# Performance work log

Hardware: AMD Instinct MI355X
Metric: run time of the kernel (lower is better)

## Reference

```python
import jax, jax.numpy as jnp
import numpy as np

N = 100000   # nodes
E = 1200000  # edges
G = 512      # graphs in batch
H = 64       # hidden_dim
EED = 8      # edge_emb_dim
VOCABS = (120, 10, 7, 5, 2)
EDIMS = (64, 16, 8, 8, 4)
BN_EPS = 1e-5


def _lin(x, w, b):
    # torch nn.Linear: y = x @ W^T + b
    return x @ w.T + b


def setup_inputs() -> dict:
    key = jax.random.key(0)
    ks = iter(jax.random.split(key, 64))
    s = 0.02
    d = {}
    d["x"] = jax.random.randint(next(ks), (N, 5), 0, 120)
    d["edge_index"] = jax.random.randint(next(ks), (2, E), 0, N)
    d["edge_attr"] = jax.random.randint(next(ks), (E, 3), 0, 16)
    d["batch"] = jnp.sort(jax.random.randint(next(ks), (N,), 0, G))
    for i, (v, dd) in enumerate(zip(VOCABS, EDIMS)):
        d[f"emb{i}"] = jax.random.normal(next(ks), (v, dd), jnp.float32) * s
    d["proj_w"] = jax.random.normal(next(ks), (H, sum(EDIMS)), jnp.float32) * s
    d["proj_b"] = jnp.zeros((H,), jnp.float32)
    for i in (1, 2, 3):
        d[f"eemb{i}"] = jax.random.normal(next(ks), (16, EED), jnp.float32) * s
        d[f"lin_e{i}_w"] = jax.random.normal(next(ks), (H, EED), jnp.float32) * s
        d[f"lin_e{i}_b"] = jnp.zeros((H,), jnp.float32)
        d[f"eps{i}"] = jnp.zeros((), jnp.float32)
        d[f"mlp{i}_w1"] = jax.random.normal(next(ks), (H, H), jnp.float32) * s
        d[f"mlp{i}_b1"] = jnp.zeros((H,), jnp.float32)
        d[f"mlp{i}_w2"] = jax.random.normal(next(ks), (H, H), jnp.float32) * s
        d[f"mlp{i}_b2"] = jnp.zeros((H,), jnp.float32)
    d["bn_g"] = jnp.ones((H,), jnp.float32)
    d["bn_b"] = jnp.zeros((H,), jnp.float32)
    d["bn_rm"] = jnp.zeros((H,), jnp.float32)
    d["bn_rv"] = jnp.ones((H,), jnp.float32)
    d["gate_w"] = jax.random.normal(next(ks), (1, H), jnp.float32) * s
    d["gate_b"] = jnp.zeros((1,), jnp.float32)
    d["head_w1"] = jax.random.normal(next(ks), (128, H), jnp.float32) * s
    d["head_b1"] = jnp.zeros((128,), jnp.float32)
    d["head_w2"] = jax.random.normal(next(ks), (1, 128), jnp.float32) * s
    d["head_b2"] = jnp.zeros((1,), jnp.float32)
    return d


def reference(x, edge_index, edge_attr, batch,
              emb0, emb1, emb2, emb3, emb4, proj_w, proj_b,
              eemb1, lin_e1_w, lin_e1_b, eps1, mlp1_w1, mlp1_b1, mlp1_w2, mlp1_b2,
              eemb2, lin_e2_w, lin_e2_b, eps2, mlp2_w1, mlp2_b1, mlp2_w2, mlp2_b2,
              eemb3, lin_e3_w, lin_e3_b, eps3, mlp3_w1, mlp3_b1, mlp3_w2, mlp3_b2,
              bn_g, bn_b, bn_rm, bn_rv, gate_w, gate_b,
              head_w1, head_b1, head_w2, head_b2):
    # --- node embedding lookup (clamped per-table, as in torch) ---
    tabs = [emb0, emb1, emb2, emb3, emb4]
    feats = [t[jnp.clip(x[:, i], 0, t.shape[0] - 1)] for i, t in enumerate(tabs)]
    h = jnp.concatenate(feats, axis=-1)            # [N, 100]
    h = _lin(h, proj_w, proj_b)                    # [N, H]  (dropout = identity, eval)

    # --- edge hash, shared by all blocks ---
    eh = (edge_attr[:, 0] + 3 * edge_attr[:, 1] + 7 * edge_attr[:, 2]) % 16  # [E]
    src, dst = edge_index[0], edge_index[1]

    def gine(h, eemb, lw, lb, eps, w1, b1, w2, b2):
        # GINEConv: mlp((1+eps) x_i + sum_j relu(x_j + lin(e_ij)))
        e = _lin(eemb[eh], lw, lb)                        # [E, H]
        msg = jax.nn.relu(h[src] + e)                     # [E, H] gather + combine
        agg = jax.ops.segment_sum(msg, dst, num_segments=N)  # scatter-add to targets
        z = (1.0 + eps) * h + agg
        return _lin(jax.nn.relu(_lin(z, w1, b1)), w2, b2)

    h = jax.nn.relu(gine(h, eemb1, lin_e1_w, lin_e1_b, eps1, mlp1_w1, mlp1_b1, mlp1_w2, mlp1_b2))
    h = jax.nn.relu(gine(h, eemb2, lin_e2_w, lin_e2_b, eps2, mlp2_w1, mlp2_b1, mlp2_w2, mlp2_b2))
    h = jax.nn.relu(gine(h, eemb3, lin_e3_w, lin_e3_b, eps3, mlp3_w1, mlp3_b1, mlp3_w2, mlp3_b2))

    # BatchNorm1d (eval mode, running stats)
    h = (h - bn_rm) * jax.lax.rsqrt(bn_rv + BN_EPS) * bn_g + bn_b

    # AttentionalAggregation: segment softmax over gate, weighted segment sum
    gate = _lin(h, gate_w, gate_b)[:, 0]                  # [N]
    m = jax.ops.segment_max(gate, batch, num_segments=G)  # [G]
    w = jnp.exp(gate - m[batch])
    den = jax.ops.segment_sum(w, batch, num_segments=G) + 1e-16
    alpha = w / den[batch]                                # [N]
    graph = jax.ops.segment_sum(alpha[:, None] * h, batch, num_segments=G)  # [G, H]

    out = _lin(jax.nn.relu(_lin(graph, head_w1, head_b1)), head_w2, head_b2)  # [G, 1]
    return out[:, 0]
```

## Files before the change

kernel.cpp:

```cpp
#include <hip/hip_runtime.h>
#include <stdint.h>

#define N_NODES 100000
#define N_EDGES 1200000
#define N_GRAPH 512
#define HID 64

#define NBUCK 391
#define BCAP  4096
#define CHUNK 4096

#define PRE_JOBS (144 * 64 + 3 * 1024 + 64 + NBUCK)

__device__ __forceinline__ unsigned short f2bf(float f) {
    unsigned u = __float_as_uint(f);
    u += 0x7FFF + ((u >> 16) & 1);
    return (unsigned short)(u >> 16);
}
__device__ __forceinline__ float bf2f(unsigned short b) {
    return __uint_as_float((unsigned)b << 16);
}

__global__ __launch_bounds__(256) void k_pre(
    const float* emb0, const float* emb1, const float* emb2, const float* emb3, const float* emb4,
    const float* proj_w,
    const float* ee1, const float* lw1, const float* lb1,
    const float* ee2, const float* lw2, const float* lb2,
    const float* ee3, const float* lw3, const float* lb3,
    const float* bn_g, const float* bn_b, const float* bn_rm, const float* bn_rv,
    float* ptab, float* elin, float* bnsc, float* bnsh, int* cursor)
{
    int job = blockIdx.x * 256 + threadIdx.x;
    if (job < 144 * 64) {
        int row = job >> 6, c = job & 63;
        const float* emb; int lr, dim, off;
        if (row < 120)      { emb = emb0; lr = row;       dim = 64; off = 0;  }
        else if (row < 130) { emb = emb1; lr = row - 120; dim = 16; off = 64; }
        else if (row < 137) { emb = emb2; lr = row - 130; dim = 8;  off = 80; }
        else if (row < 142) { emb = emb3; lr = row - 137; dim = 8;  off = 88; }
        else                { emb = emb4; lr = row - 142; dim = 4;  off = 96; }
        float s = 0.f;
        for (int d = 0; d < dim; ++d)
            s += emb[lr * dim + d] * proj_w[c * 100 + off + d];
        ptab[row * 64 + c] = s;
    } else if (job < 144 * 64 + 3 * 1024) {
        int j = job - 144 * 64;
        int L = j >> 10; int r = (j >> 6) & 15; int c = j & 63;
        const float* ee = (L == 0) ? ee1 : (L == 1) ? ee2 : ee3;
        const float* lw = (L == 0) ? lw1 : (L == 1) ? lw2 : lw3;
        const float* lb = (L == 0) ? lb1 : (L == 1) ? lb2 : lb3;
        float s = lb[c];
        for (int d = 0; d < 8; ++d) s += ee[r * 8 + d] * lw[c * 8 + d];
        elin[j] = s;
    } else if (job < 144 * 64 + 3 * 1024 + 64) {
        int c = job - (144 * 64 + 3 * 1024);
        float sc = bn_g[c] * rsqrtf(bn_rv[c] + 1e-5f);
        bnsc[c] = sc;
        bnsh[c] = bn_b[c] - bn_rm[c] * sc;
    } else if (job < PRE_JOBS) {
        cursor[job - (144 * 64 + 3 * 1024 + 64)] = 0;
    }
}

__global__ __launch_bounds__(256) void k_embed(const int* x, const float* ptab,
                                               const float* proj_b, float* h,
                                               unsigned short* h2) {
    int id = blockIdx.x * 256 + threadIdx.x;
    if (id >= N_NODES * HID) return;
    int n = id >> 6, c = id & 63;
    const int* xr = x + n * 5;
    int r0 = min(max(xr[0], 0), 119);
    int r1 = 120 + min(max(xr[1], 0), 9);
    int r2 = 130 + min(max(xr[2], 0), 6);
    int r3 = 137 + min(max(xr[3], 0), 4);
    int r4 = 142 + min(max(xr[4], 0), 1);
    float v = proj_b[c] + ptab[r0 * 64 + c] + ptab[r1 * 64 + c] + ptab[r2 * 64 + c]
            + ptab[r3 * 64 + c] + ptab[r4 * 64 + c];
    h[id] = v;
    h2[id] = f2bf(v);
}

__global__ __launch_bounds__(256) void k_gptr(const int* batch, int* gptr) {
    int n = blockIdx.x * 256 + threadIdx.x;
    if (n >= N_NODES) return;
    int b = batch[n];
    int bp = (n == 0) ? -1 : batch[n - 1];
    for (int g = bp + 1; g <= b; ++g) gptr[g] = n;
    if (n == N_NODES - 1) {
        for (int g = b + 1; g <= N_GRAPH; ++g) gptr[g] = N_NODES;
    }
}

__global__ __launch_bounds__(256) void k_bin(const int* __restrict__ ei,
                                             const int* __restrict__ ea,
                                             int* __restrict__ cursor,
                                             int* __restrict__ binned) {
    __shared__ int pay[CHUNK];
    __shared__ unsigned short bkid[CHUNK];
    __shared__ int hist[NBUCK], inc[NBUCK], tmp[NBUCK], gdelta[NBUCK];
    int t = threadIdx.x;
    int e0 = blockIdx.x * CHUNK;
    for (int i = t; i < NBUCK; i += 256) hist[i] = 0;
    __syncthreads();
    int mypay[16], myrb[16];
    #pragma unroll
    for (int j = 0; j < 16; ++j) {
        int e = e0 + j * 256 + t;
        myrb[j] = -1;
        if (e < N_EDGES) {
            int s = ei[e];
            int d = ei[N_EDGES + e];
            int hsh = (ea[e * 3] + 3 * ea[e * 3 + 1] + 7 * ea[e * 3 + 2]) & 15;
            int b = d >> 8;
            mypay[j] = s | (hsh << 17) | ((d & 255) << 21);
            int r = atomicAdd(&hist[b], 1);
            myrb[j] = r | (b << 12);
        }
    }
    __syncthreads();
    for (int i = t; i < NBUCK; i += 256) inc[i] = hist[i];
    __syncthreads();
    for (int off = 1; off < NBUCK; off <<= 1) {
        for (int i = t; i < NBUCK; i += 256) tmp[i] = inc[i] + ((i >= off) ? inc[i - off] : 0);
        __syncthreads();
        for (int i = t; i < NBUCK; i += 256) inc[i] = tmp[i];
        __syncthreads();
    }
    for (int i = t; i < NBUCK; i += 256) {
        int c = hist[i];
        int gp = c ? atomicAdd(&cursor[i], c) : 0;
        gdelta[i] = i * BCAP + gp - (inc[i] - c);
    }
    __syncthreads();
    #pragma unroll
    for (int j = 0; j < 16; ++j) {
        if (myrb[j] >= 0) {
            int b = myrb[j] >> 12, r = myrb[j] & 0xFFF;
            int slot = (inc[b] - hist[b]) + r;
            pay[slot] = mypay[j];
            bkid[slot] = (unsigned short)b;
        }
    }
    __syncthreads();
    int tot = inc[NBUCK - 1];
    for (int i = t; i < tot; i += 256)
        binned[gdelta[bkid[i]] + i] = pay[i];
}

__global__ __launch_bounds__(512) void k_bscan(const int* cursor, int* bbase, int* rowptr) {
    __shared__ int s[512], tp[512];
    int t = threadIdx.x;
    int v = (t < NBUCK) ? cursor[t] : 0;
    s[t] = v;
    __syncthreads();
    for (int off = 1; off < 512; off <<= 1) {
        tp[t] = s[t] + ((t >= off) ? s[t - off] : 0);
        __syncthreads();
        s[t] = tp[t];
        __syncthreads();
    }
    if (t < NBUCK) bbase[t] = s[t] - v;
    if (t == 0) { bbase[NBUCK] = N_EDGES; rowptr[N_NODES] = N_EDGES; }
}

__global__ __launch_bounds__(256) void k_fin(const int* __restrict__ binned,
                                             const int* __restrict__ cursor,
                                             const int* __restrict__ bbase,
                                             int* __restrict__ rowptr,
                                             int* __restrict__ epk) {
    __shared__ int h2[256], sc[256], cur[256];
    int b = blockIdx.x, t = threadIdx.x;
    int cnt = cursor[b];
    int gb = bbase[b];
    int node0 = b << 8;
    h2[t] = 0;
    __syncthreads();
    const int* bp = binned + b * BCAP;
    for (int i = t; i < cnt; i += 256) atomicAdd(&h2[(bp[i] >> 21) & 255], 1);
    __syncthreads();
    sc[t] = h2[t];
    __syncthreads();
    for (int off = 1; off < 256; off <<= 1) {
        int v = (t >= off) ? sc[t - off] : 0;
        __syncthreads();
        sc[t] += v;
        __syncthreads();
    }
    int ex = sc[t] - h2[t];
    cur[t] = ex;
    int n = node0 + t;
    if (n < N_NODES) rowptr[n] = gb + ex;
    __syncthreads();
    for (int i = t; i < cnt; i += 256) {
        int p = bp[i];
        int pos = atomicAdd(&cur[(p >> 21) & 255], 1);
        epk[gb + pos] = p & 0x1FFFFF;
    }
}

__global__ __launch_bounds__(256) void k_gather(const unsigned short* __restrict__ h2,
                                                const float* __restrict__ elinL,
                                                const int* __restrict__ rowptr,
                                                const int* __restrict__ epk,
                                                float* __restrict__ agg) {
    __shared__ float es[16 * 64];
    int t = threadIdx.x;
    ((float4*)es)[t] = ((const float4*)elinL)[t];
    __syncthreads();
    int n = blockIdx.x * 4 + (t >> 6);
    if (n >= N_NODES) return;
    int lane = t & 63;
    int grp = lane >> 4;
    int c4 = (lane & 15) << 2;
    int p0 = rowptr[n], p1 = rowptr[n + 1];
    float4 acc = make_float4(0.f, 0.f, 0.f, 0.f);
    int p = p0 + grp;
    while (p + 4 < p1) {
        int pk0 = epk[p];
        int pk1 = epk[p + 4];
        ushort4 a0 = *(const ushort4*)(h2 + (pk0 & 0x1FFFF) * 64 + c4);
        ushort4 a1 = *(const ushort4*)(h2 + (pk1 & 0x1FFFF) * 64 + c4);
        float4 e0 = *(const float4*)(es + ((pk0 >> 17) & 15) * 64 + c4);
        float4 e1 = *(const float4*)(es + ((pk1 >> 17) & 15) * 64 + c4);
        acc.x += fmaxf(bf2f(a0.x) + e0.x, 0.f) + fmaxf(bf2f(a1.x) + e1.x, 0.f);
        acc.y += fmaxf(bf2f(a0.y) + e0.y, 0.f) + fmaxf(bf2f(a1.y) + e1.y, 0.f);
        acc.z += fmaxf(bf2f(a0.z) + e0.z, 0.f) + fmaxf(bf2f(a1.z) + e1.z, 0.f);
        acc.w += fmaxf(bf2f(a0.w) + e0.w, 0.f) + fmaxf(bf2f(a1.w) + e1.w, 0.f);
        p += 8;
    }
    if (p < p1) {
        int pk0 = epk[p];
        ushort4 a0 = *(const ushort4*)(h2 + (pk0 & 0x1FFFF) * 64 + c4);
        float4 e0 = *(const float4*)(es + ((pk0 >> 17) & 15) * 64 + c4);
        acc.x += fmaxf(bf2f(a0.x) + e0.x, 0.f);
        acc.y += fmaxf(bf2f(a0.y) + e0.y, 0.f);
        acc.z += fmaxf(bf2f(a0.z) + e0.z, 0.f);
        acc.w += fmaxf(bf2f(a0.w) + e0.w, 0.f);
    }
    acc.x += __shfl_down(acc.x, 32, 64);
    acc.y += __shfl_down(acc.y, 32, 64);
    acc.z += __shfl_down(acc.z, 32, 64);
    acc.w += __shfl_down(acc.w, 32, 64);
    acc.x += __shfl_down(acc.x, 16, 64);
    acc.y += __shfl_down(acc.y, 16, 64);
    acc.z += __shfl_down(acc.z, 16, 64);
    acc.w += __shfl_down(acc.w, 16, 64);
    if (grp == 0) *(float4*)(agg + n * 64 + c4) = acc;
}

__global__ __launch_bounds__(256) void k_mlp2(const float* __restrict__ hin,
                                              const float* __restrict__ agg,
                                              const float* __restrict__ epsp,
                                              const float* __restrict__ W1,
                                              const float* __restrict__ b1,
                                              const float* __restrict__ W2,
                                              const float* __restrict__ b2,
                                              float* __restrict__ out,
                                              unsigned short* __restrict__ h2out,
                                              const float* __restrict__ bnsc,
                                              const float* __restrict__ bnsh,
                                              const float* __restrict__ gate_w,
                                              const float* __restrict__ gate_b,
                                              float* __restrict__ gate) {
    __shared__ float in_s[64 * 68];
    __shared__ float wt_s[64 * 68];
    int t = threadIdx.x;
    int row0 = blockIdx.x * 64;
    float epsv = 1.f + epsp[0];
    for (int idx = t; idx < 1024; idx += 256) {
        int r = idx >> 4, cc4 = (idx & 15) << 2;
        int gr = row0 + r;
        float4 v = make_float4(0.f, 0.f, 0.f, 0.f);
        if (gr < N_NODES) {
            float4 a = *(const float4*)(hin + gr * 64 + cc4);
            float4 b = *(const float4*)(agg + gr * 64 + cc4);
            v.x = epsv * a.x + b.x; v.y = epsv * a.y + b.y;
            v.z = epsv * a.z + b.z; v.w = epsv * a.w + b.w;
        }
        *(float4*)(in_s + r * 68 + cc4) = v;
    }
    for (int idx = t; idx < 1024; idx += 256) {
        int cc = idx >> 4, k4 = (idx & 15) << 2;
        float4 w = *(const float4*)(W1 + cc * 64 + k4);
        wt_s[(k4 + 0) * 68 + cc] = w.x;
        wt_s[(k4 + 1) * 68 + cc] = w.y;
        wt_s[(k4 + 2) * 68 + cc] = w.z;
        wt_s[(k4 + 3) * 68 + cc] = w.w;
    }
    __syncthreads();
    int tc = t & 15, tr = t >> 4;
    float acc[4][4] = {};
    for (int k4 = 0; k4 < 16; ++k4) {
        float4 a[4], b[4];
        #pragma unroll
        for (int i = 0; i < 4; ++i) a[i] = *(float4*)(in_s + (tr + 16 * i) * 68 + k4 * 4);
        #pragma unroll
        for (int kk = 0; kk < 4; ++kk) b[kk] = *(float4*)(wt_s + (k4 * 4 + kk) * 68 + tc * 4);
        #pragma unroll
        for (int i = 0; i < 4; ++i) {
            float ax = a[i].x, ay = a[i].y, az = a[i].z, aw = a[i].w;
            acc[i][0] += ax * b[0].x + ay * b[1].x + az * b[2].x + aw * b[3].x;
            acc[i][1] += ax * b[0].y + ay * b[1].y + az * b[2].y + aw * b[3].y;
            acc[i][2] += ax * b[0].z + ay * b[1].z + az * b[2].z + aw * b[3].z;
            acc[i][3] += ax * b[0].w + ay * b[1].w + az * b[2].w + aw * b[3].w;
        }
    }
    __syncthreads();
    {
        float4 bb1 = *(const float4*)(b1 + tc * 4);
        #pragma unroll
        for (int i = 0; i < 4; ++i) {
            float* row = in_s + (tr + 16 * i) * 68 + tc * 4;
            row[0] = fmaxf(acc[i][0] + bb1.x, 0.f);
            row[1] = fmaxf(acc[i][1] + bb1.y, 0.f);
            row[2] = fmaxf(acc[i][2] + bb1.z, 0.f);
            row[3] = fmaxf(acc[i][3] + bb1.w, 0.f);
        }
    }
    for (int idx = t; idx < 1024; idx += 256) {
        int cc = idx >> 4, k4 = (idx & 15) << 2;
        float4 w = *(const float4*)(W2 + cc * 64 + k4);
        wt_s[(k4 + 0) * 68 + cc] = w.x;
        wt_s[(k4 + 1) * 68 + cc] = w.y;
        wt_s[(k4 + 2) * 68 + cc] = w.z;
        wt_s[(k4 + 3) * 68 + cc] = w.w;
    }
    __syncthreads();
    float acc2[4][4] = {};
    for (int k4 = 0; k4 < 16; ++k4) {
        float4 a[4], b[4];
        #pragma unroll
        for (int i = 0; i < 4; ++i) a[i] = *(float4*)(in_s + (tr + 16 * i) * 68 + k4 * 4);
        #pragma unroll
        for (int kk = 0; kk < 4; ++kk) b[kk] = *(float4*)(wt_s + (k4 * 4 + kk) * 68 + tc * 4);
        #pragma unroll
        for (int i = 0; i < 4; ++i) {
            float ax = a[i].x, ay = a[i].y, az = a[i].z, aw = a[i].w;
            acc2[i][0] += ax * b[0].x + ay * b[1].x + az * b[2].x + aw * b[3].x;
            acc2[i][1] += ax * b[0].y + ay * b[1].y + az * b[2].y + aw * b[3].y;
            acc2[i][2] += ax * b[0].z + ay * b[1].z + az * b[2].z + aw * b[3].z;
            acc2[i][3] += ax * b[0].w + ay * b[1].w + az * b[2].w + aw * b[3].w;
        }
    }
    float4 bb2 = *(const float4*)(b2 + tc * 4);
    if (gate == nullptr) {
        #pragma unroll
        for (int i = 0; i < 4; ++i) {
            int gr = row0 + tr + 16 * i;
            if (gr < N_NODES) {
                float4 o;
                o.x = fmaxf(acc2[i][0] + bb2.x, 0.f);
                o.y = fmaxf(acc2[i][1] + bb2.y, 0.f);
                o.z = fmaxf(acc2[i][2] + bb2.z, 0.f);
                o.w = fmaxf(acc2[i][3] + bb2.w, 0.f);
                *(float4*)(out + gr * 64 + tc * 4) = o;
                ushort4 ob;
                ob.x = f2bf(o.x); ob.y = f2bf(o.y); ob.z = f2bf(o.z); ob.w = f2bf(o.w);
                *(ushort4*)(h2out + gr * 64 + tc * 4) = ob;
            }
        }
    } else {
        float4 sc = *(const float4*)(bnsc + tc * 4);
        float4 sh = *(const float4*)(bnsh + tc * 4);
        float4 gw = *(const float4*)(gate_w + tc * 4);
        float gb = gate_b[0];
        #pragma unroll
        for (int i = 0; i < 4; ++i) {
            int gr = row0 + tr + 16 * i;
            float4 o;
            o.x = fmaxf(acc2[i][0] + bb2.x, 0.f) * sc.x + sh.x;
            o.y = fmaxf(acc2[i][1] + bb2.y, 0.f) * sc.y + sh.y;
            o.z = fmaxf(acc2[i][2] + bb2.z, 0.f) * sc.z + sh.z;
            o.w = fmaxf(acc2[i][3] + bb2.w, 0.f) * sc.w + sh.w;
            float p = o.x * gw.x + o.y * gw.y + o.z * gw.z + o.w * gw.w;
            p += __shfl_down(p, 8, 16);
            p += __shfl_down(p, 4, 16);
            p += __shfl_down(p, 2, 16);
            p += __shfl_down(p, 1, 16);
            if (gr < N_NODES) {
                *(float4*)(out + gr * 64 + tc * 4) = o;
                if (tc == 0) gate[gr] = p + gb;
            }
        }
    }
}

__global__ __launch_bounds__(256) void k_att(const float* __restrict__ h,
                                             const float* __restrict__ gate,
                                             const int* __restrict__ gptr,
                                             float* __restrict__ graph) {
    __shared__ float red[4];
    __shared__ float acc_s[4][64];
    __shared__ float m_s, den_s;
    int t = threadIdx.x, g = blockIdx.x;
    int n0 = gptr[g], n1 = gptr[g + 1];
    float m = -INFINITY;
    for (int n = n0 + t; n < n1; n += 256) m = fmaxf(m, gate[n]);
    #pragma unroll
    for (int off = 32; off > 0; off >>= 1) m = fmaxf(m, __shfl_down(m, off, 64));
    if ((t & 63) == 0) red[t >> 6] = m;
    __syncthreads();
    if (t == 0) m_s = fmaxf(fmaxf(red[0], red[1]), fmaxf(red[2], red[3]));
    __syncthreads();
    m = m_s;
    float s = 0.f;
    for (int n = n0 + t; n < n1; n += 256) s += expf(gate[n] - m);
    #pragma unroll
    for (int off = 32; off > 0; off >>= 1) s += __shfl_down(s, off, 64);
    if ((t & 63) == 0) red[t >> 6] = s;
    __syncthreads();
    if (t == 0) den_s = red[0] + red[1] + red[2] + red[3] + 1e-16f;
    __syncthreads();
    float invden = 1.f / den_s;
    int c = t & 63, w = t >> 6;
    float acc = 0.f;
    for (int n = n0 + w; n < n1; n += 4) {
        float a = expf(gate[n] - m);
        acc += a * h[n * 64 + c];
    }
    acc_s[w][c] = acc;
    __syncthreads();
    if (w == 0)
        graph[g * 64 + c] = (acc_s[0][c] + acc_s[1][c] + acc_s[2][c] + acc_s[3][c]) * invden;
}

__global__ __launch_bounds__(128) void k_head(const float* graph, const float* w1, const float* b1,
                                              const float* w2, const float* b2, float* out) {
    __shared__ float w1s[128 * 65];
    __shared__ float gs[64];
    __shared__ float red[2];
    int t = threadIdx.x, g = blockIdx.x;
    for (int idx = t; idx < 128 * 16; idx += 128) {
        int r = idx >> 4, c4 = (idx & 15) << 2;
        float4 v = *(const float4*)(w1 + r * 64 + c4);
        w1s[r * 65 + c4 + 0] = v.x;
        w1s[r * 65 + c4 + 1] = v.y;
        w1s[r * 65 + c4 + 2] = v.z;
        w1s[r * 65 + c4 + 3] = v.w;
    }
    if (t < 64) gs[t] = graph[g * 64 + t];
    __syncthreads();
    float s = b1[t];
    #pragma unroll
    for (int k = 0; k < 64; ++k) s += gs[k] * w1s[t * 65 + k];
    float p = fmaxf(s, 0.f) * w2[t];
    #pragma unroll
    for (int off = 32; off > 0; off >>= 1) p += __shfl_down(p, off, 64);
    if ((t & 63) == 0) red[t >> 6] = p;
    __syncthreads();
    if (t == 0) out[g] = red[0] + red[1] + b2[0];
}

extern "C" void kernel_launch(void* const* d_in, const int* in_sizes, int n_in,
                              void* d_out, int out_size, void* d_ws, size_t ws_size,
                              hipStream_t stream) {
    const int* x    = (const int*)d_in[0];
    const int* ei   = (const int*)d_in[1];
    const int* ea   = (const int*)d_in[2];
    const int* bat  = (const int*)d_in[3];
    const float* emb0 = (const float*)d_in[4];
    const float* emb1 = (const float*)d_in[5];
    const float* emb2 = (const float*)d_in[6];
    const float* emb3 = (const float*)d_in[7];
    const float* emb4 = (const float*)d_in[8];
    const float* proj_w = (const float*)d_in[9];
    const float* proj_b = (const float*)d_in[10];
    const float* bn_g  = (const float*)d_in[35];
    const float* bn_b  = (const float*)d_in[36];
    const float* bn_rm = (const float*)d_in[37];
    const float* bn_rv = (const float*)d_in[38];
    const float* gate_w = (const float*)d_in[39];
    const float* gate_b = (const float*)d_in[40];
    const float* head_w1 = (const float*)d_in[41];
    const float* head_b1 = (const float*)d_in[42];
    const float* head_w2 = (const float*)d_in[43];
    const float* head_b2 = (const float*)d_in[44];

    char* wsb = (char*)d_ws;
    size_t o = 0;
    auto alloc = [&](size_t bytes) -> void* {
        void* p = wsb + o;
        o += (bytes + 255) & ~(size_t)255;
        return p;
    };
    float* ptab   = (float*)alloc(144 * 64 * 4);
    float* elin   = (float*)alloc(3 * 16 * 64 * 4);
    float* bnsc   = (float*)alloc(64 * 4);
    float* bnsh   = (float*)alloc(64 * 4);
    int* cursor   = (int*)alloc(NBUCK * 4);
    int* bbase    = (int*)alloc((NBUCK + 1) * 4);
    int* gptr     = (int*)alloc((N_GRAPH + 1) * 4);
    int* rowptr   = (int*)alloc(((size_t)N_NODES + 1) * 4);
    int* binned   = (int*)alloc((size_t)NBUCK * BCAP * 4);
    int* epk      = (int*)alloc((size_t)N_EDGES * 4);
    float* h      = (float*)alloc((size_t)N_NODES * 64 * 4);
    unsigned short* h2 = (unsigned short*)alloc((size_t)N_NODES * 64 * 2);
    float* agg    = (float*)alloc((size_t)N_NODES * 64 * 4);
    float* gate   = (float*)alloc((size_t)N_NODES * 4);
    float* graph  = (float*)alloc((size_t)N_GRAPH * 64 * 4);

    k_pre<<<(PRE_JOBS + 255) / 256, 256, 0, stream>>>(
                                  emb0, emb1, emb2, emb3, emb4, proj_w,
                                  (const float*)d_in[11], (const float*)d_in[12], (const float*)d_in[13],
                                  (const float*)d_in[19], (const float*)d_in[20], (const float*)d_in[21],
                                  (const float*)d_in[27], (const float*)d_in[28], (const float*)d_in[29],
                                  bn_g, bn_b, bn_rm, bn_rv,
                                  ptab, elin, bnsc, bnsh, cursor);
    k_embed<<<(N_NODES * 64 + 255) / 256, 256, 0, stream>>>(x, ptab, proj_b, h, h2);
    k_gptr<<<(N_NODES + 255) / 256, 256, 0, stream>>>(bat, gptr);
    k_bin<<<(N_EDGES + CHUNK - 1) / CHUNK, 256, 0, stream>>>(ei, ea, cursor, binned);
    k_bscan<<<1, 512, 0, stream>>>(cursor, bbase, rowptr);
    k_fin<<<NBUCK, 256, 0, stream>>>(binned, cursor, bbase, rowptr, epk);

    for (int L = 0; L < 3; ++L) {
        const float* epsp = (const float*)d_in[14 + L * 8];
        const float* w1   = (const float*)d_in[15 + L * 8];
        const float* b1   = (const float*)d_in[16 + L * 8];
        const float* w2   = (const float*)d_in[17 + L * 8];
        const float* b2   = (const float*)d_in[18 + L * 8];
        k_gather<<<(N_NODES + 3) / 4, 256, 0, stream>>>(h2, elin + L * 1024, rowptr, epk, agg);
        if (L < 2) {
            k_mlp2<<<(N_NODES + 63) / 64, 256, 0, stream>>>(h, agg, epsp, w1, b1, w2, b2, h, h2,
                                                            nullptr, nullptr, nullptr, nullptr,
                                                            nullptr);
        } else {
            k_mlp2<<<(N_NODES + 63) / 64, 256, 0, stream>>>(h, agg, epsp, w1, b1, w2, b2, h, nullptr,
                                                            bnsc, bnsh, gate_w, gate_b, gate);
        }
    }

    k_att<<<N_GRAPH, 256, 0, stream>>>(h, gate, gptr, graph);
    k_head<<<N_GRAPH, 128, 0, stream>>>(graph, head_w1, head_b1, head_w2, head_b2, (float*)d_out);
}
```

Before: 474.4 us.

## Use bf16 MFMA for GIN MLPs, pre-convert weights, fuse head into attention

The per-layer two-layer MLP kernel is rewritten to use bf16 MFMA 16x16x32 instructions. Weights are converted to bf16 once in the prep kernel and held in registers, and the intermediate activations are staged in LDS as bf16. This replaces the fp32 FMA tiling and the weight transposes into shared memory. The separate head kernel is also folded into the attention pooling kernel to save a launch. The cost is lower precision in the MLP inputs and hidden activations, plus uncoalesced scalar output stores.

Result: faster. 445.3 us (-6.1%).

```diff
diff --git a/kernel.cpp b/kernel.cpp
--- a/kernel.cpp
+++ b/kernel.cpp
@@ -10,7 +10,11 @@
 #define BCAP  4096
 #define CHUNK 4096
 
-#define PRE_JOBS (144 * 64 + 3 * 1024 + 64 + NBUCK)
+#define PRE_W0  (144 * 64 + 3 * 1024 + 64 + NBUCK)
+#define PRE_JOBS (PRE_W0 + 6 * 4096)
+
+typedef __attribute__((ext_vector_type(8))) short bshort8;
+typedef __attribute__((ext_vector_type(4))) float f32x4;
 
 __device__ __forceinline__ unsigned short f2bf(float f) {
     unsigned u = __float_as_uint(f);
@@ -28,7 +32,10 @@
     const float* ee2, const float* lw2, const float* lb2,
     const float* ee3, const float* lw3, const float* lb3,
     const float* bn_g, const float* bn_b, const float* bn_rm, const float* bn_rv,
-    float* ptab, float* elin, float* bnsc, float* bnsh, int* cursor)
+    const float* w11, const float* w12, const float* w21, const float* w22,
+    const float* w31, const float* w32,
+    float* ptab, float* elin, float* bnsc, float* bnsh, int* cursor,
+    unsigned short* wbf)
 {
     int job = blockIdx.x * 256 + threadIdx.x;
     if (job < 144 * 64) {
@@ -57,8 +64,14 @@
         float sc = bn_g[c] * rsqrtf(bn_rv[c] + 1e-5f);
         bnsc[c] = sc;
         bnsh[c] = bn_b[c] - bn_rm[c] * sc;
+    } else if (job < PRE_W0) {
+        cursor[job - (144 * 64 + 3 * 1024 + 64)] = 0;
     } else if (job < PRE_JOBS) {
-        cursor[job - (144 * 64 + 3 * 1024 + 64)] = 0;
+        int j2 = job - PRE_W0;
+        int sel = j2 >> 12;
+        const float* W = (sel == 0) ? w11 : (sel == 1) ? w12 : (sel == 2) ? w21
+                       : (sel == 3) ? w22 : (sel == 4) ? w31 : w32;
+        wbf[j2] = f2bf(W[j2 & 4095]);
     }
 }
 
@@ -248,12 +261,12 @@
     if (grp == 0) *(float4*)(agg + n * 64 + c4) = acc;
 }
 
-__global__ __launch_bounds__(256) void k_mlp2(const float* __restrict__ hin,
+__global__ __launch_bounds__(256) void k_mlpm(const float* __restrict__ hin,
                                               const float* __restrict__ agg,
                                               const float* __restrict__ epsp,
-                                              const float* __restrict__ W1,
+                                              const unsigned short* __restrict__ wbf1,
                                               const float* __restrict__ b1,
-                                              const float* __restrict__ W2,
+                                              const unsigned short* __restrict__ wbf2,
                                               const float* __restrict__ b2,
                                               float* __restrict__ out,
                                               unsigned short* __restrict__ h2out,
@@ -262,125 +275,100 @@
                                               const float* __restrict__ gate_w,
                                               const float* __restrict__ gate_b,
                                               float* __restrict__ gate) {
-    __shared__ float in_s[64 * 68];
-    __shared__ float wt_s[64 * 68];
+    __shared__ unsigned short zb[64 * 72];
+    __shared__ unsigned short hb[64 * 72];
     int t = threadIdx.x;
     int row0 = blockIdx.x * 64;
     float epsv = 1.f + epsp[0];
     for (int idx = t; idx < 1024; idx += 256) {
-        int r = idx >> 4, cc4 = (idx & 15) << 2;
+        int r = idx >> 4, c4 = (idx & 15) << 2;
         int gr = row0 + r;
         float4 v = make_float4(0.f, 0.f, 0.f, 0.f);
         if (gr < N_NODES) {
-            float4 a = *(const float4*)(hin + gr * 64 + cc4);
-            float4 b = *(const float4*)(agg + gr * 64 + cc4);
+            float4 a = *(const float4*)(hin + gr * 64 + c4);
+            float4 b = *(const float4*)(agg + gr * 64 + c4);
             v.x = epsv * a.x + b.x; v.y = epsv * a.y + b.y;
             v.z = epsv * a.z + b.z; v.w = epsv * a.w + b.w;
         }
-        *(float4*)(in_s + r * 68 + cc4) = v;
-    }
-    for (int idx = t; idx < 1024; idx += 256) {
-        int cc = idx >> 4, k4 = (idx & 15) << 2;
-        float4 w = *(const float4*)(W1 + cc * 64 + k4);
-        wt_s[(k4 + 0) * 68 + cc] = w.x;
-        wt_s[(k4 + 1) * 68 + cc] = w.y;
-        wt_s[(k4 + 2) * 68 + cc] = w.z;
-        wt_s[(k4 + 3) * 68 + cc] = w.w;
-    }
-    __syncthreads();
-    int tc = t & 15, tr = t >> 4;
-    float acc[4][4] = {};
-    for (int k4 = 0; k4 < 16; ++k4) {
-        float4 a[4], b[4];
+        ushort4 zv;
+        zv.x = f2bf(v.x); zv.y = f2bf(v.y); zv.z = f2bf(v.z); zv.w = f2bf(v.w);
+        *(ushort4*)(zb + r * 72 + c4) = zv;
+    }
+    int lane = t & 63, wv = t >> 6;
+    int quad = lane >> 4, lc = lane & 15;
+    int m0 = wv * 16;
+    bshort8 w1f[4][2];
+    #pragma unroll
+    for (int nt = 0; nt < 4; ++nt)
         #pragma unroll
-        for (int i = 0; i < 4; ++i) a[i] = *(float4*)(in_s + (tr + 16 * i) * 68 + k4 * 4);
+        for (int kt = 0; kt < 2; ++kt)
+            w1f[nt][kt] = *(const bshort8*)(wbf1 + (nt * 16 + lc) * 64 + kt * 32 + quad * 8);
+    bshort8 w2f[4][2];
+    #pragma unroll
+    for (int nt = 0; nt < 4; ++nt)
         #pragma unroll
-        for (int kk = 0; kk < 4; ++kk) b[kk] = *(float4*)(wt_s + (k4 * 4 + kk) * 68 + tc * 4);
+        for (int kt = 0; kt < 2; ++kt)
+            w2f[nt][kt] = *(const bshort8*)(wbf2 + (nt * 16 + lc) * 64 + kt * 32 + quad * 8);
+    __syncthreads();
+    bshort8 a0 = *(const bshort8*)(zb + (m0 + lc) * 72 + quad * 8);
+    bshort8 a1 = *(const bshort8*)(zb + (m0 + lc) * 72 + 32 + quad * 8);
+    f32x4 acc1[4];
+    #pragma unroll
+    for (int nt = 0; nt < 4; ++nt) {
+        acc1[nt] = (f32x4){0.f, 0.f, 0.f, 0.f};
+        acc1[nt] = __builtin_amdgcn_mfma_f32_16x16x32_bf16(a0, w1f[nt][0], acc1[nt], 0, 0, 0);
+        acc1[nt] = __builtin_amdgcn_mfma_f32_16x16x32_bf16(a1, w1f[nt][1], acc1[nt], 0, 0, 0);
+    }
+    #pragma unroll
+    for (int nt = 0; nt < 4; ++nt) {
+        float bb = b1[nt * 16 + lc];
         #pragma unroll
-        for (int i = 0; i < 4; ++i) {
-            float ax = a[i].x, ay = a[i].y, az = a[i].z, aw = a[i].w;
-            acc[i][0] += ax * b[0].x + ay * b[1].x + az * b[2].x + aw * b[3].x;
-            acc[i][1] += ax * b[0].y + ay * b[1].y + az * b[2].y + aw * b[3].y;
-            acc[i][2] += ax * b[0].z + ay * b[1].z + az * b[2].z + aw * b[3].z;
-            acc[i][3] += ax * b[0].w + ay * b[1].w + az * b[2].w + aw * b[3].w;
-        }
-    }
-    __syncthreads();
-    {
-        float4 bb1 = *(const float4*)(b1 + tc * 4);
-        #pragma unroll
-        for (int i = 0; i < 4; ++i) {
-            float* row = in_s + (tr + 16 * i) * 68 + tc * 4;
-            row[0] = fmaxf(acc[i][0] + bb1.x, 0.f);
-            row[1] = fmaxf(acc[i][1] + bb1.y, 0.f);
-            row[2] = fmaxf(acc[i][2] + bb1.z, 0.f);
-            row[3] = fmaxf(acc[i][3] + bb1.w, 0.f);
-        }
-    }
-    for (int idx = t; idx < 1024; idx += 256) {
-        int cc = idx >> 4, k4 = (idx & 15) << 2;
-        float4 w = *(const float4*)(W2 + cc * 64 + k4);
-        wt_s[(k4 + 0) * 68 + cc] = w.x;
-        wt_s[(k4 + 1) * 68 + cc] = w.y;
-        wt_s[(k4 + 2) * 68 + cc] = w.z;
-        wt_s[(k4 + 3) * 68 + cc] = w.w;
-    }
-    __syncthreads();
-    float acc2[4][4] = {};
-    for (int k4 = 0; k4 < 16; ++k4) {
-        float4 a[4], b[4];
-        #pragma unroll
-        for (int i = 0; i < 4; ++i) a[i] = *(float4*)(in_s + (tr + 16 * i) * 68 + k4 * 4);
-        #pragma unroll
-        for (int kk = 0; kk < 4; ++kk) b[kk] = *(float4*)(wt_s + (k4 * 4 + kk) * 68 + tc * 4);
-        #pragma unroll
-        for (int i = 0; i < 4; ++i) {
-            float ax = a[i].x, ay = a[i].y, az = a[i].z, aw = a[i].w;
-            acc2[i][0] += ax * b[0].x + ay * b[1].x + az * b[2].x + aw * b[3].x;
-            acc2[i][1] += ax * b[0].y + ay * b[1].y + az * b[2].y + aw * b[3].y;
-            acc2[i][2] += ax * b[0].z + ay * b[1].z + az * b[2].z + aw * b[3].z;
-            acc2[i][3] += ax * b[0].w + ay * b[1].w + az * b[2].w + aw * b[3].w;
-        }
-    }
-    float4 bb2 = *(const float4*)(b2 + tc * 4);
+        for (int reg = 0; reg < 4; ++reg) {
+            float v = fmaxf(acc1[nt][reg] + bb, 0.f);
+            hb[(m0 + quad * 4 + reg) * 72 + nt * 16 + lc] = f2bf(v);
+        }
+    }
+    bshort8 c0 = *(const bshort8*)(hb + (m0 + lc) * 72 + quad * 8);
+    bshort8 c1 = *(const bshort8*)(hb + (m0 + lc) * 72 + 32 + quad * 8);
+    f32x4 acc2[4];
+    #pragma unroll
+    for (int nt = 0; nt < 4; ++nt) {
+        acc2[nt] = (f32x4){0.f, 0.f, 0.f, 0.f};
+        acc2[nt] = __builtin_amdgcn_mfma_f32_16x16x32_bf16(c0, w2f[nt][0], acc2[nt], 0, 0, 0);
+        acc2[nt] = __builtin_amdgcn_mfma_f32_16x16x32_bf16(c1, w2f[nt][1], acc2[nt], 0, 0, 0);
+    }
     if (gate == nullptr) {
         #pragma unroll
-        for (int i = 0; i < 4; ++i) {
-            int gr = row0 + tr + 16 * i;
+        for (int reg = 0; reg < 4; ++reg) {
+            int gr = row0 + m0 + quad * 4 + reg;
             if (gr < N_NODES) {
-                float4 o;
-                o.x = fmaxf(acc2[i][0] + bb2.x, 0.f);
-                o.y = fmaxf(acc2[i][1] + bb2.y, 0.f);
-                o.z = fmaxf(acc2[i][2] + bb2.z, 0.f);
-                o.w = fmaxf(acc2[i][3] + bb2.w, 0.f);
-                *(float4*)(out + gr * 64 + tc * 4) = o;
-                ushort4 ob;
-                ob.x = f2bf(o.x); ob.y = f2bf(o.y); ob.z = f2bf(o.z); ob.w = f2bf(o.w);
-                *(ushort4*)(h2out + gr * 64 + tc * 4) = ob;
+                #pragma unroll
+                for (int nt = 0; nt < 4; ++nt) {
+                    int col = nt * 16 + lc;
+                    float v = fmaxf(acc2[nt][reg] + b2[col], 0.f);
+                    out[gr * 64 + col] = v;
+                    h2out[gr * 64 + col] = f2bf(v);
+                }
             }
         }
     } else {
-        float4 sc = *(const float4*)(bnsc + tc * 4);
-        float4 sh = *(const float4*)(bnsh + tc * 4);
-        float4 gw = *(const float4*)(gate_w + tc * 4);
         float gb = gate_b[0];
         #pragma unroll
-        for (int i = 0; i < 4; ++i) {
-            int gr = row0 + tr + 16 * i;
-            float4 o;
-            o.x = fmaxf(acc2[i][0] + bb2.x, 0.f) * sc.x + sh.x;
-            o.y = fmaxf(acc2[i][1] + bb2.y, 0.f) * sc.y + sh.y;
-            o.z = fmaxf(acc2[i][2] + bb2.z, 0.f) * sc.z + sh.z;
-            o.w = fmaxf(acc2[i][3] + bb2.w, 0.f) * sc.w + sh.w;
-            float p = o.x * gw.x + o.y * gw.y + o.z * gw.z + o.w * gw.w;
+        for (int reg = 0; reg < 4; ++reg) {
+            int gr = row0 + m0 + quad * 4 + reg;
+            float p = 0.f;
+            #pragma unroll
+            for (int nt = 0; nt < 4; ++nt) {
+                int col = nt * 16 + lc;
+                float v = fmaxf(acc2[nt][reg] + b2[col], 0.f) * bnsc[col] + bnsh[col];
+                p += v * gate_w[col];
+                if (gr < N_NODES) out[gr * 64 + col] = v;
+            }
             p += __shfl_down(p, 8, 16);
             p += __shfl_down(p, 4, 16);
             p += __shfl_down(p, 2, 16);
             p += __shfl_down(p, 1, 16);
-            if (gr < N_NODES) {
-                *(float4*)(out + gr * 64 + tc * 4) = o;
-                if (tc == 0) gate[gr] = p + gb;
-            }
+            if (lc == 0 && gr < N_NODES) gate[gr] = p + gb;
         }
     }
 }
@@ -388,9 +376,14 @@
 __global__ __launch_bounds__(256) void k_att(const float* __restrict__ h,
                                              const float* __restrict__ gate,
                                              const int* __restrict__ gptr,
-                                             float* __restrict__ graph) {
+                                             const float* __restrict__ hw1,
+                                             const float* __restrict__ hb1,
+                                             const float* __restrict__ hw2,
+                                             const float* __restrict__ hb2,
+                                             float* __restrict__ out) {
     __shared__ float red[4];
     __shared__ float acc_s[4][64];
+    __shared__ float gvec[64];
     __shared__ float m_s, den_s;
     int t = threadIdx.x, g = blockIdx.x;
     int n0 = gptr[g], n1 = gptr[g + 1];
@@ -421,34 +414,22 @@
     acc_s[w][c] = acc;
     __syncthreads();
     if (w == 0)
-        graph[g * 64 + c] = (acc_s[0][c] + acc_s[1][c] + acc_s[2][c] + acc_s[3][c]) * invden;
-}
-
-__global__ __launch_bounds__(128) void k_head(const float* graph, const float* w1, const float* b1,
-                                              const float* w2, const float* b2, float* out) {
-    __shared__ float w1s[128 * 65];
-    __shared__ float gs[64];
-    __shared__ float red[2];
-    int t = threadIdx.x, g = blockIdx.x;
-    for (int idx = t; idx < 128 * 16; idx += 128) {
-        int r = idx >> 4, c4 = (idx & 15) << 2;
-        float4 v = *(const float4*)(w1 + r * 64 + c4);
-        w1s[r * 65 + c4 + 0] = v.x;
-        w1s[r * 65 + c4 + 1] = v.y;
-        w1s[r * 65 + c4 + 2] = v.z;
-        w1s[r * 65 + c4 + 3] = v.w;
-    }
-    if (t < 64) gs[t] = graph[g * 64 + t];
-    __syncthreads();
-    float s = b1[t];
-    #pragma unroll
-    for (int k = 0; k < 64; ++k) s += gs[k] * w1s[t * 65 + k];
-    float p = fmaxf(s, 0.f) * w2[t];
+        gvec[c] = (acc_s[0][c] + acc_s[1][c] + acc_s[2][c] + acc_s[3][c]) * invden;
+    __syncthreads();
+    float p = 0.f;
+    if (t < 128) {
+        float sh = hb1[t];
+        const float* wr = hw1 + t * 64;
+        #pragma unroll
+        for (int k = 0; k < 64; ++k) sh += gvec[k] * wr[k];
+        p = fmaxf(sh, 0.f) * hw2[t];
+    }
     #pragma unroll
     for (int off = 32; off > 0; off >>= 1) p += __shfl_down(p, off, 64);
-    if ((t & 63) == 0) red[t >> 6] = p;
-    __syncthreads();
-    if (t == 0) out[g] = red[0] + red[1] + b2[0];
+    if (t == 0) red[0] = p;
+    if (t == 64) red[1] = p;
+    __syncthreads();
+    if (t == 0) out[g] = red[0] + red[1] + hb2[0];
 }
 
 extern "C" void kernel_launch(void* const* d_in, const int* in_sizes, int n_in,
@@ -497,7 +478,7 @@
     unsigned short* h2 = (unsigned short*)alloc((size_t)N_NODES * 64 * 2);
     float* agg    = (float*)alloc((size_t)N_NODES * 64 * 4);
     float* gate   = (float*)alloc((size_t)N_NODES * 4);
-    float* graph  = (float*)alloc((size_t)N_GRAPH * 64 * 4);
+    unsigned short* wbf = (unsigned short*)alloc(6 * 4096 * 2);
 
     k_pre<<<(PRE_JOBS + 255) / 256, 256, 0, stream>>>(
                                   emb0, emb1, emb2, emb3, emb4, proj_w,
@@ -505,7 +486,10 @@
                                   (const float*)d_in[19], (const float*)d_in[20], (const float*)d_in[21],
                                   (const float*)d_in[27], (const float*)d_in[28], (const float*)d_in[29],
                                   bn_g, bn_b, bn_rm, bn_rv,
-                                  ptab, elin, bnsc, bnsh, cursor);
+                                  (const float*)d_in[15], (const float*)d_in[17],
+                                  (const float*)d_in[23], (const float*)d_in[25],
+                                  (const float*)d_in[31], (const float*)d_in[33],
+                                  ptab, elin, bnsc, bnsh, cursor, wbf);
     k_embed<<<(N_NODES * 64 + 255) / 256, 256, 0, stream>>>(x, ptab, proj_b, h, h2);
     k_gptr<<<(N_NODES + 255) / 256, 256, 0, stream>>>(bat, gptr);
     k_bin<<<(N_EDGES + CHUNK - 1) / CHUNK, 256, 0, stream>>>(ei, ea, cursor, binned);
@@ -514,21 +498,21 @@
 
     for (int L = 0; L < 3; ++L) {
         const float* epsp = (const float*)d_in[14 + L * 8];
-        const float* w1   = (const float*)d_in[15 + L * 8];
         const float* b1   = (const float*)d_in[16 + L * 8];
-        const float* w2   = (const float*)d_in[17 + L * 8];
         const float* b2   = (const float*)d_in[18 + L * 8];
+        const unsigned short* wb1 = wbf + (L * 2 + 0) * 4096;
+        const unsigned short* wb2 = wbf + (L * 2 + 1) * 4096;
         k_gather<<<(N_NODES + 3) / 4, 256, 0, stream>>>(h2, elin + L * 1024, rowptr, epk, agg);
         if (L < 2) {
-            k_mlp2<<<(N_NODES + 63) / 64, 256, 0, stream>>>(h, agg, epsp, w1, b1, w2, b2, h, h2,
+            k_mlpm<<<(N_NODES + 63) / 64, 256, 0, stream>>>(h, agg, epsp, wb1, b1, wb2, b2, h, h2,
                                                             nullptr, nullptr, nullptr, nullptr,
                                                             nullptr);
         } else {
-            k_mlp2<<<(N_NODES + 63) / 64, 256, 0, stream>>>(h, agg, epsp, w1, b1, w2, b2, h, nullptr,
+            k_mlpm<<<(N_NODES + 63) / 64, 256, 0, stream>>>(h, agg, epsp, wb1, b1, wb2, b2, h, nullptr,
                                                             bnsc, bnsh, gate_w, gate_b, gate);
         }
     }
 
-    k_att<<<N_GRAPH, 256, 0, stream>>>(h, gate, gptr, graph);
-    k_head<<<N_GRAPH, 128, 0, stream>>>(graph, head_w1, head_b1, head_w2, head_b2, (float*)d_out);
-}
+    k_att<<<N_GRAPH, 256, 0, stream>>>(h, gate, gptr, head_w1, head_b1, head_w2, head_b2,
+                                       (float*)d_out);
+}
```
